# Kernel tuning notes

Measured on AMD Instinct MI355X. Metric: run time of the kernel, lower is better.

Reference implementation:

```python
import jax, jax.numpy as jnp
import numpy as np

B, F, DEPTH = 8192, 256, 6

def entmax15(x):
    # exact 1.5-entmax along the last axis (sort-based algorithm)
    x = x / 2.0
    x = x - jnp.max(x, axis=-1, keepdims=True)
    xs = -jnp.sort(-x, axis=-1)                      # descending sort
    d = x.shape[-1]
    rho = jnp.arange(1, d + 1, dtype=x.dtype)
    mean = jnp.cumsum(xs, axis=-1) / rho
    mean_sq = jnp.cumsum(xs * xs, axis=-1) / rho
    ss = rho * (mean_sq - mean * mean)
    tau = mean - jnp.sqrt(jnp.clip((1.0 - ss) / rho, 0.0))
    support = jnp.sum((tau <= xs).astype(jnp.int32), axis=-1)
    tau_star = jnp.take_along_axis(tau, (support - 1)[..., None], axis=-1)
    return jnp.square(jnp.clip(x - tau_star, 0.0))

def _stump_level(x_in, fm, cp, lr):
    # x_in: [B,Fd]; fm: [n,Fd]; cp,lr: [n,Fd,2]. Vectorized over all n stumps of a level.
    mask = entmax15(fm)                                      # [n,Fd] feature gating
    w = jnp.array([1.0, 2.0], dtype=x_in.dtype)              # cutpoint-bin weights W
    z = entmax15(x_in[None, :, :, None] * w - cp[:, None])   # [n,B,Fd,2] binning
    out = jnp.einsum('nbfl,nfl,nf->nbl', z, lr, mask)        # leaf responses, masked sum over features
    # torch.cat of per-stump [B,2] along dim=1 -> [B, n*2]
    return jnp.transpose(out, (1, 0, 2)).reshape(x_in.shape[0], -1), mask

def _forward(x, params):
    tree_input = x
    masks = []
    out = None
    for fm, cp, lr in params:
        out, m = _stump_level(tree_input, fm, cp, lr)
        tree_input = jnp.concatenate([x, out], axis=1)
        masks.append(m)
    return out, masks

def setup_inputs() -> dict:
    key = jax.random.key(0)
    ks = jax.random.split(key, 1 + 3 * DEPTH)
    inp = {"x": jax.random.normal(ks[0], (B, F), dtype=jnp.float32)}
    for d in range(DEPTH):
        n = 2 ** d
        Fd = F + (2 ** d if d > 0 else 0)
        inp[f"fm{d}"] = jax.random.uniform(ks[1 + 3 * d], (n, Fd), dtype=jnp.float32)
        inp[f"cp{d}"] = jax.random.uniform(ks[2 + 3 * d], (n, Fd, 2), dtype=jnp.float32)
        inp[f"lr{d}"] = jax.random.uniform(ks[3 + 3 * d], (n, Fd, 2), dtype=jnp.float32)
    return inp

def reference(x, fm0, cp0, lr0, fm1, cp1, lr1, fm2, cp2, lr2, fm3, cp3, lr3, fm4, cp4, lr4, fm5, cp5, lr5):
    params = [(fm0, cp0, lr0), (fm1, cp1, lr1), (fm2, cp2, lr2),
              (fm3, cp3, lr3), (fm4, cp4, lr4), (fm5, cp5, lr5)]
    out, masks = _forward(x, params)  # dropout=0 -> identity
    return (out, *masks)
```

## Files before the change

kernel.cpp:

```cpp
#include <hip/hip_runtime.h>

#define B_SZ 8192


struct MaskArgs {
  const float* fm[6];
  const float* cp[6];
  const float* lr[6];
  float* out_masks;
  float4* cprm;
  int* cnt;
  float* cstf;
};

__device__ __forceinline__ float wave_max(float v) {
#pragma unroll
  for (int o = 32; o > 0; o >>= 1) v = fmaxf(v, __shfl_xor(v, o));
  return v;
}
__device__ __forceinline__ float wave_sum(float v) {
#pragma unroll
  for (int o = 32; o > 0; o >>= 1) v += __shfl_xor(v, o);
  return v;
}

__global__ __launch_bounds__(64) void ndt_masks(MaskArgs a) {
  const int maskOff[6] = {524288, 524544, 525060, 526100, 528212, 532564};
  const int prmOff[6]  = {0, 256, 772, 1812, 3924, 8276};
  const int cstOff[6]  = {0, 1, 3, 7, 15, 31};
  const int exBase[6]  = {0, 256, 258, 262, 270, 286};
  int bid = blockIdx.x, lane = threadIdx.x;
  int d = 0, s = bid, n = 1;
  while (s >= n) { s -= n; n <<= 1; ++d; }
  int Fd = 256 + ((d > 0) ? n : 0);

  const float* fm = a.fm[d] + (size_t)s * Fd;
  float y[5];
#pragma unroll
  for (int j = 0; j < 5; ++j) {
    int f = lane + 64 * j;
    y[j] = (f < Fd) ? fm[f] * 0.5f : -3.0e38f;
  }
  float m = fmaxf(fmaxf(fmaxf(y[0], y[1]), fmaxf(y[2], y[3])), y[4]);
  m = wave_max(m);
#pragma unroll
  for (int j = 0; j < 5; ++j) y[j] -= m;

  float lo = -1.f, hi = 0.f;
  for (int it = 0; it < 24; ++it) {
    float tau = 0.5f * (lo + hi);
    float ss = 0.f;
#pragma unroll
    for (int j = 0; j < 5; ++j) {
      float v = fmaxf(y[j] - tau, 0.f);
      ss = __builtin_fmaf(v, v, ss);
    }
    ss = wave_sum(ss);
    if (ss >= 1.f) lo = tau; else hi = tau;
  }
  float tau = 0.5f * (lo + hi);

  float* mo = a.out_masks + maskOff[d] + (size_t)s * Fd;
  const float* cp = a.cp[d] + (size_t)s * Fd * 2;
  const float* lr = a.lr[d] + (size_t)s * Fd * 2;
  float4* cpr = a.cprm + prmOff[d] + (size_t)s * Fd;
  int exB = exBase[d];
  float sum0 = 0.f, sum1 = 0.f;
  int base = 0;
#pragma unroll
  for (int j = 0; j < 5; ++j) {
    int f = lane + 64 * j;
    bool in = (f < Fd);
    float v = fmaxf(y[j] - tau, 0.f);
    float mk = v * v;
    float c10 = 0.f, ml0 = 0.f, ml1 = 0.f;
    if (in) {
      mo[f] = mk;
      float c0 = cp[2 * f], c1 = cp[2 * f + 1];
      ml0 = lr[2 * f] * mk;
      ml1 = lr[2 * f + 1] * mk;
      c10 = c1 - c0;
      sum0 += ml0;
      sum1 += ml1;
    }
    bool act = in && (v > 0.f);
    unsigned long long bm = __ballot(act);
    int pre = __popcll(bm & ((1ull << lane) - 1ull));
    if (act) {
      int fidx = (f < 256) ? f : (exB + f - 256);
      cpr[base + pre] =
          make_float4(c10, ml0 * 0.125f, ml1 * 0.125f, __int_as_float(fidx));
    }
    base += __popcll(bm);
  }
  sum0 = wave_sum(sum0);
  sum1 = wave_sum(sum1);
  if (lane == 0) {
    a.cstf[2 * (cstOff[d] + s)] = 0.5f * sum0;
    a.cstf[2 * (cstOff[d] + s) + 1] = 0.5f * sum1;
    a.cnt[cstOff[d] + s] = base;
  }
}

__device__ __forceinline__ float entpair(float c10, float xv) {
  float t = c10 - xv;
  float tc = __builtin_amdgcn_fmed3f(t, -2.f, 2.f);
  float u = __builtin_fmaf(tc, -tc, 8.0f);
  return tc * __builtin_amdgcn_sqrtf(u);
}

template <int N, int FD>
__device__ __forceinline__ void ndt_level(const float4* __restrict__ cp,
                                          const int* __restrict__ cN,
                                          const float* __restrict__ cs,
                                          int outRow, int g, int l,
                                          float* __restrict__ xls,
                                          float (*__restrict__ pbuf)[2][16]) {
  constexpr int SPG = 32 / N;
  int s = g / SPG, slice = g - s * SPG;
  int nc = cN[s];
  const float4* ps = cp + (size_t)s * FD;
  float a0 = 0.f, a1 = 0.f;
  int jlo = slice * nc / SPG, jhi = (slice + 1) * nc / SPG;
#pragma unroll 4
  for (int j = jlo; j < jhi; ++j) {
    float4 p = ps[j];
    int row = __float_as_int(p.w);
    float xv = xls[row * 17 + l];
    float e = entpair(p.x, xv);
    a0 = __builtin_fmaf(e, p.y, a0);
    a1 = __builtin_fmaf(-e, p.z, a1);
  }
  pbuf[g][0][l] = a0;
  pbuf[g][1][l] = a1;
  __syncthreads();
  for (int o = g; o < 2 * N; o += 32) {
    int s2 = o >> 1, par = o & 1;
    float v = cs[o];
#pragma unroll
    for (int k = 0; k < SPG; ++k) v += pbuf[s2 * SPG + k][par][l];
    xls[(outRow + o) * 17 + l] = v;
  }
  __syncthreads();
}

__global__ __launch_bounds__(512) void ndt_all(const float* __restrict__ x,
                                               const float4* __restrict__ cprm,
                                               const int* __restrict__ cnt,
                                               const float* __restrict__ cstf,
                                               float* __restrict__ out) {
  __shared__ float xls[318 * 17];
  __shared__ float pbuf[32][2][16];
  __shared__ float fres[64 * 17];
  int tid = threadIdx.x;
  int g = tid >> 4, l = tid & 15;
  int b0 = blockIdx.x * 16;
  {
    int c = tid >> 5, seg = tid & 31;
    const float4* xp = (const float4*)(x + (size_t)(b0 + c) * 256 + seg * 8);
    float4 v0 = xp[0], v1 = xp[1];
    int f = seg * 8;
    xls[(f + 0) * 17 + c] = v0.x;
    xls[(f + 1) * 17 + c] = v0.y;
    xls[(f + 2) * 17 + c] = v0.z;
    xls[(f + 3) * 17 + c] = v0.w;
    xls[(f + 4) * 17 + c] = v1.x;
    xls[(f + 5) * 17 + c] = v1.y;
    xls[(f + 6) * 17 + c] = v1.z;
    xls[(f + 7) * 17 + c] = v1.w;
  }
  __syncthreads();
  ndt_level<1, 256>(cprm, cnt, cstf, 256, g, l, xls, pbuf);
  ndt_level<2, 258>(cprm + 256, cnt + 1, cstf + 2, 258, g, l, xls, pbuf);
  ndt_level<4, 260>(cprm + 772, cnt + 3, cstf + 6, 262, g, l, xls, pbuf);
  ndt_level<8, 264>(cprm + 1812, cnt + 7, cstf + 14, 270, g, l, xls, pbuf);
  ndt_level<16, 272>(cprm + 3924, cnt + 15, cstf + 30, 286, g, l, xls, pbuf);
  {
    const float4* cp5 = cprm + 8276;
    int nc = cnt[31 + g];
    const float4* ps = cp5 + (size_t)g * 288;
    float a0 = cstf[62 + 2 * g], a1 = cstf[62 + 2 * g + 1];
#pragma unroll 4
    for (int j = 0; j < nc; ++j) {
      float4 p = ps[j];
      int row = __float_as_int(p.w);
      float xv = xls[row * 17 + l];
      float e = entpair(p.x, xv);
      a0 = __builtin_fmaf(e, p.y, a0);
      a1 = __builtin_fmaf(-e, p.z, a1);
    }
    fres[(2 * g) * 17 + l] = a0;
    fres[(2 * g + 1) * 17 + l] = a1;
  }
  __syncthreads();
  {
    int c = tid >> 5, o = (tid & 31) * 2;
    float2 v = make_float2(fres[o * 17 + c], fres[(o + 1) * 17 + c]);
    *(float2*)(out + (size_t)(b0 + c) * 64 + o) = v;
  }
}

extern "C" void kernel_launch(void* const* d_in, const int* in_sizes, int n_in,
                              void* d_out, int out_size, void* d_ws, size_t ws_size,
                              hipStream_t stream) {
  const float* x = (const float*)d_in[0];
  float* out = (float*)d_out;
  float* wsf = (float*)d_ws;

  float4* cprm = (float4*)(wsf + 2575872);
  float* cstf = wsf + 2645840;
  int* cnt = (int*)(wsf + 2645966);

  MaskArgs ma;
  for (int d = 0; d < 6; ++d) {
    ma.fm[d] = (const float*)d_in[1 + 3 * d];
    ma.cp[d] = (const float*)d_in[2 + 3 * d];
    ma.lr[d] = (const float*)d_in[3 + 3 * d];
  }
  ma.out_masks = out;
  ma.cprm = cprm;
  ma.cnt = cnt;
  ma.cstf = cstf;
  hipLaunchKernelGGL(ndt_masks, dim3(63), dim3(64), 0, stream, ma);

  hipLaunchKernelGGL(ndt_all, dim3(B_SZ / 16), dim3(512), 0, stream,
                     x, cprm, cnt, cstf, out);
}
```

Baseline: 45.53 us.

## Halve rows per block to 8 and split each stump across 64 groups

Each block now handles 8 batch rows instead of 16, with 64 groups of 8 lanes, so each stump's active-feature list is split across twice as many slices. The grid doubles to 1024 blocks and LDS per block shrinks, and launch bounds request higher occupancy. The last level now goes through the generic split-and-reduce path and writes its output through the shared x buffer, which drops the separate fres stage. In exchange, every cutpoint parameter is reloaded by twice as many blocks, each float4 load feeds only 8 lanes, and the final store is scalar rather than float2.

```diff
diff --git a/kernel.cpp b/kernel.cpp
--- a/kernel.cpp
+++ b/kernel.cpp
@@ -115,8 +115,8 @@
                                           const float* __restrict__ cs,
                                           int outRow, int g, int l,
                                           float* __restrict__ xls,
-                                          float (*__restrict__ pbuf)[2][16]) {
-  constexpr int SPG = 32 / N;
+                                          float (*__restrict__ pbuf)[2][8]) {
+  constexpr int SPG = 64 / N;
   int s = g / SPG, slice = g - s * SPG;
   int nc = cN[s];
   const float4* ps = cp + (size_t)s * FD;
@@ -126,7 +126,7 @@
   for (int j = jlo; j < jhi; ++j) {
     float4 p = ps[j];
     int row = __float_as_int(p.w);
-    float xv = xls[row * 17 + l];
+    float xv = xls[row * 9 + l];
     float e = entpair(p.x, xv);
     a0 = __builtin_fmaf(e, p.y, a0);
     a1 = __builtin_fmaf(-e, p.z, a1);
@@ -134,40 +134,34 @@
   pbuf[g][0][l] = a0;
   pbuf[g][1][l] = a1;
   __syncthreads();
-  for (int o = g; o < 2 * N; o += 32) {
+  for (int o = g; o < 2 * N; o += 64) {
     int s2 = o >> 1, par = o & 1;
     float v = cs[o];
 #pragma unroll
     for (int k = 0; k < SPG; ++k) v += pbuf[s2 * SPG + k][par][l];
-    xls[(outRow + o) * 17 + l] = v;
+    xls[(outRow + o) * 9 + l] = v;
   }
   __syncthreads();
 }
 
-__global__ __launch_bounds__(512) void ndt_all(const float* __restrict__ x,
-                                               const float4* __restrict__ cprm,
-                                               const int* __restrict__ cnt,
-                                               const float* __restrict__ cstf,
-                                               float* __restrict__ out) {
-  __shared__ float xls[318 * 17];
-  __shared__ float pbuf[32][2][16];
-  __shared__ float fres[64 * 17];
+__global__ __launch_bounds__(512, 8) void ndt_all(const float* __restrict__ x,
+                                                  const float4* __restrict__ cprm,
+                                                  const int* __restrict__ cnt,
+                                                  const float* __restrict__ cstf,
+                                                  float* __restrict__ out) {
+  __shared__ float xls[382 * 9];
+  __shared__ float pbuf[64][2][8];
   int tid = threadIdx.x;
-  int g = tid >> 4, l = tid & 15;
-  int b0 = blockIdx.x * 16;
+  int g = tid >> 3, l = tid & 7;
+  int b0 = blockIdx.x * 8;
   {
-    int c = tid >> 5, seg = tid & 31;
-    const float4* xp = (const float4*)(x + (size_t)(b0 + c) * 256 + seg * 8);
-    float4 v0 = xp[0], v1 = xp[1];
-    int f = seg * 8;
-    xls[(f + 0) * 17 + c] = v0.x;
-    xls[(f + 1) * 17 + c] = v0.y;
-    xls[(f + 2) * 17 + c] = v0.z;
-    xls[(f + 3) * 17 + c] = v0.w;
-    xls[(f + 4) * 17 + c] = v1.x;
-    xls[(f + 5) * 17 + c] = v1.y;
-    xls[(f + 6) * 17 + c] = v1.z;
-    xls[(f + 7) * 17 + c] = v1.w;
+    int c = tid >> 6, seg = tid & 63;
+    float4 v = *(const float4*)(x + (size_t)(b0 + c) * 256 + seg * 4);
+    int f = seg * 4;
+    xls[(f + 0) * 9 + c] = v.x;
+    xls[(f + 1) * 9 + c] = v.y;
+    xls[(f + 2) * 9 + c] = v.z;
+    xls[(f + 3) * 9 + c] = v.w;
   }
   __syncthreads();
   ndt_level<1, 256>(cprm, cnt, cstf, 256, g, l, xls, pbuf);
@@ -175,28 +169,10 @@
   ndt_level<4, 260>(cprm + 772, cnt + 3, cstf + 6, 262, g, l, xls, pbuf);
   ndt_level<8, 264>(cprm + 1812, cnt + 7, cstf + 14, 270, g, l, xls, pbuf);
   ndt_level<16, 272>(cprm + 3924, cnt + 15, cstf + 30, 286, g, l, xls, pbuf);
+  ndt_level<32, 288>(cprm + 8276, cnt + 31, cstf + 62, 318, g, l, xls, pbuf);
   {
-    const float4* cp5 = cprm + 8276;
-    int nc = cnt[31 + g];
-    const float4* ps = cp5 + (size_t)g * 288;
-    float a0 = cstf[62 + 2 * g], a1 = cstf[62 + 2 * g + 1];
-#pragma unroll 4
-    for (int j = 0; j < nc; ++j) {
-      float4 p = ps[j];
-      int row = __float_as_int(p.w);
-      float xv = xls[row * 17 + l];
-      float e = entpair(p.x, xv);
-      a0 = __builtin_fmaf(e, p.y, a0);
-      a1 = __builtin_fmaf(-e, p.z, a1);
-    }
-    fres[(2 * g) * 17 + l] = a0;
-    fres[(2 * g + 1) * 17 + l] = a1;
-  }
-  __syncthreads();
-  {
-    int c = tid >> 5, o = (tid & 31) * 2;
-    float2 v = make_float2(fres[o * 17 + c], fres[(o + 1) * 17 + c]);
-    *(float2*)(out + (size_t)(b0 + c) * 64 + o) = v;
+    int c = tid >> 6, o = tid & 63;
+    out[(size_t)(b0 + c) * 64 + o] = xls[(318 + o) * 9 + c];
   }
 }
 
@@ -223,6 +199,6 @@
   ma.cstf = cstf;
   hipLaunchKernelGGL(ndt_masks, dim3(63), dim3(64), 0, stream, ma);
 
-  hipLaunchKernelGGL(ndt_all, dim3(B_SZ / 16), dim3(512), 0, stream,
+  hipLaunchKernelGGL(ndt_all, dim3(B_SZ / 8), dim3(512), 0, stream,
                      x, cprm, cnt, cstf, out);
 }
```

New measurement: 44.18 us. 3.0% less time.
